# Kernel tuning notes

Hardware: AMD Instinct MI355X
Metric: run time of the kernel (lower is better)

Reference implementation:

```python
import jax, jax.numpy as jnp
import numpy as np

HEADS = 8
DIM_HEAD = 64
BATCH = 2  # classifier-free-guidance batch
LORA_SCALE = 1.0


def setup_inputs() -> dict:
    key = jax.random.key(0)
    ks = jax.random.split(key, 14)
    D, R = 512, 4
    BF, N = 32, 1024  # batch*frames, spatial tokens
    g = lambda k, shape, s: jax.random.normal(k, shape, dtype=jnp.float32) * s
    return {
        "hidden_states": g(ks[0], (BF, N, D), 1.0),
        "Wq": g(ks[1], (D, D), 0.02),
        "Wk": g(ks[2], (D, D), 0.02),
        "Wv": g(ks[3], (D, D), 0.02),
        "q_down": g(ks[4], (D, R), 0.25),
        "q_up": g(ks[5], (R, D), 0.02),
        "k_down": g(ks[6], (D, R), 0.25),
        "k_up": g(ks[7], (R, D), 0.02),
        "v_down": g(ks[8], (D, R), 0.25),
        "v_up": g(ks[9], (R, D), 0.02),
        "Wo": g(ks[10], (D, D), 0.02),
        "bo": jnp.zeros((D,), jnp.float32),
        "o_down": g(ks[11], (D, R), 0.25),
        "o_up": g(ks[12], (R, D), 0.02),
    }


def reference(hidden_states, Wq, Wk, Wv, q_down, q_up, k_down, k_up,
              v_down, v_up, Wo, bo, o_down, o_up):
    BF, N, C = hidden_states.shape
    F = BF // BATCH  # video_length
    inner = HEADS * DIM_HEAD

    # LoRA-augmented QKV projections (self-attention: context == hidden_states)
    q = hidden_states @ Wq + LORA_SCALE * ((hidden_states @ q_down) @ q_up)
    k = hidden_states @ Wk + LORA_SCALE * ((hidden_states @ k_down) @ k_up)
    v = hidden_states @ Wv + LORA_SCALE * ((hidden_states @ v_down) @ v_up)

    # previous-frame gather: frame f attends to frame max(f-1, 0)
    prev = jnp.concatenate([jnp.zeros((1,), jnp.int32),
                            jnp.arange(F - 1, dtype=jnp.int32)])
    k = k.reshape(BATCH, F, N, inner)[:, prev].reshape(BF, N, inner)
    v = v.reshape(BATCH, F, N, inner)[:, prev].reshape(BF, N, inner)

    def to_heads(t):  # (BF, N, inner) -> (BF*H, N, dh)
        return t.reshape(BF, N, HEADS, DIM_HEAD).transpose(0, 2, 1, 3)\
                .reshape(BF * HEADS, N, DIM_HEAD)

    qh, kh, vh = to_heads(q), to_heads(k), to_heads(v)

    scores = jnp.einsum('bid,bjd->bij', qh, kh) * (DIM_HEAD ** -0.5)
    probs = jax.nn.softmax(scores, axis=-1)
    h = jnp.einsum('bij,bjd->bid', probs, vh)

    # heads back to channel dim
    h = h.reshape(BF, HEADS, N, DIM_HEAD).transpose(0, 2, 1, 3).reshape(BF, N, inner)

    # output projection (with bias) + LoRA on the pre-projection activations
    return h @ Wo + bo + LORA_SCALE * ((h @ o_down) @ o_up)
```

## Files before the change

### kernel.cpp

```cpp
#include <hip/hip_runtime.h>
#include <hip/hip_bf16.h>
#include <math.h>

#define D512 512
#define NTOK 1024
#define QSCALE 0.1803368801111137f

typedef __attribute__((ext_vector_type(8))) short short8;
typedef __attribute__((ext_vector_type(4))) float f32x4;
typedef __attribute__((ext_vector_type(16))) float f32x16;
typedef __attribute__((ext_vector_type(4))) unsigned int u32x4;
typedef unsigned short ushort;

__device__ inline ushort f2bf(float x) {
    union { float f; unsigned u; } a; a.f = x;
    unsigned r = a.u + 0x7FFF + ((a.u >> 16) & 1);
    return (ushort)(r >> 16);
}

__device__ inline unsigned cvtpk(float a, float b) {
    unsigned r;
    asm volatile("v_cvt_pk_bf16_f32 %0, %1, %2" : "=v"(r) : "v"(a), "v"(b));
    return r;
}

__device__ inline void plswap(unsigned &a, unsigned &b) {
    asm volatile("v_permlane32_swap_b32 %0, %1" : "+v"(a), "+v"(b));
}

#define GLL16(src, dst) __builtin_amdgcn_global_load_lds( \
    (const __attribute__((address_space(1))) unsigned int*)(src), \
    (__attribute__((address_space(3))) unsigned int*)(dst), 16, 0, 0)

__global__ __launch_bounds__(256) void cvt_bf16(
    const float* __restrict__ in, ushort* __restrict__ out)
{
    const int idx = blockIdx.x * 256 + threadIdx.x;
    float4 a = ((const float4*)in)[idx * 2];
    float4 b = ((const float4*)in)[idx * 2 + 1];
    short8 s;
    s[0] = f2bf(a.x); s[1] = f2bf(a.y); s[2] = f2bf(a.z); s[3] = f2bf(a.w);
    s[4] = f2bf(b.x); s[5] = f2bf(b.y); s[6] = f2bf(b.z); s[7] = f2bf(b.w);
    *(short8*)&out[(size_t)idx * 8] = s;
}

__global__ __launch_bounds__(256) void fold_weights_T(
    const float* __restrict__ Wq, const float* __restrict__ Wk,
    const float* __restrict__ Wv, const float* __restrict__ Wo,
    const float* __restrict__ qd, const float* __restrict__ qu,
    const float* __restrict__ kd, const float* __restrict__ ku,
    const float* __restrict__ vd, const float* __restrict__ vu,
    const float* __restrict__ od, const float* __restrict__ ou,
    ushort* __restrict__ out)
{
    const int which = blockIdx.y;
    const float *W, *dn, *up;
    if (which == 0)      { W = Wq; dn = qd; up = qu; }
    else if (which == 1) { W = Wk; dn = kd; up = ku; }
    else if (which == 2) { W = Wv; dn = vd; up = vu; }
    else                 { W = Wo; dn = od; up = ou; }

    const int td = (blockIdx.x >> 3) * 64;
    const int te = (blockIdx.x & 7) * 64;
    __shared__ float T[64][65];
    const int r4 = threadIdx.x >> 6;
    const int c  = threadIdx.x & 63;

    #pragma unroll
    for (int i = 0; i < 16; ++i) {
        int row = i * 4 + r4;
        T[row][c] = W[(size_t)(td + row) * 512 + te + c];
    }
    __syncthreads();
    #pragma unroll
    for (int i = 0; i < 16; ++i) {
        int e = te + i * 4 + r4;
        int d = td + c;
        float s = T[c][i * 4 + r4];
        #pragma unroll
        for (int r = 0; r < 4; ++r) s += dn[d * 4 + r] * up[r * 512 + e];
        out[(size_t)which * 262144 + (size_t)e * 512 + d] = f2bf(s);
    }
}

template<int QKV>
__global__ __launch_bounds__(256) void gemm_mfma(
    const ushort* __restrict__ A, const ushort* __restrict__ BT,
    const float* __restrict__ bias, float* __restrict__ Co,
    ushort* __restrict__ qb, ushort* __restrict__ kb, ushort* __restrict__ vtb)
{
    __shared__ ushort smem[16384];

    const int tid = threadIdx.x;
    const int w = tid >> 6, l = tid & 63;
    const int l15 = l & 15, l4 = l >> 4;

    const int wg = blockIdx.x;
    const int rxcd = wg & 7, t = wg >> 3;
    const int NX = QKV ? 12 : 4;
    const int xb = t % NX, yh = t / NX;
    const int yb = (yh << 3) | rxcd;
    const int m0 = yb * 128;
    const int n0 = xb * 128;

    const int srow = l >> 2;
    const int scol = (l & 3) * 8;
    const ushort* Asrc = A  + (size_t)(m0 + w * 32 + srow) * 512 + scol;
    const ushort* Bsrc = BT + (size_t)(n0 + w * 32 + srow) * 512 + scol;

    const int wm = (w >> 1) * 64, wn = (w & 1) * 64;

    f32x4 acc[4][4] = {};

    {
        ushort* AsW = smem + w * 1024;
        ushort* BsW = smem + 4096 + w * 1024;
        GLL16(Asrc, AsW);            GLL16(Asrc + 16 * 512, AsW + 512);
        GLL16(Bsrc, BsW);            GLL16(Bsrc + 16 * 512, BsW + 512);
    }
    __syncthreads();

    int cur = 0;
    for (int k0 = 0; k0 < 512; k0 += 32) {
        if (k0 < 480) {
            ushort* AsW = smem + (cur ^ 1) * 8192 + w * 1024;
            ushort* BsW = smem + (cur ^ 1) * 8192 + 4096 + w * 1024;
            GLL16(Asrc + k0 + 32, AsW);
            GLL16(Asrc + k0 + 32 + 16 * 512, AsW + 512);
            GLL16(Bsrc + k0 + 32, BsW);
            GLL16(Bsrc + k0 + 32 + 16 * 512, BsW + 512);
        }
        const ushort* As = smem + cur * 8192;
        const ushort* Bs = smem + cur * 8192 + 4096;

        short8 bfr[4];
        #pragma unroll
        for (int ni = 0; ni < 4; ++ni)
            bfr[ni] = *(const short8*)&Bs[(wn + ni * 16 + l15) * 32 + l4 * 8];
        __builtin_amdgcn_s_setprio(1);
        #pragma unroll
        for (int mi = 0; mi < 4; ++mi) {
            short8 af = *(const short8*)&As[(wm + mi * 16 + l15) * 32 + l4 * 8];
            #pragma unroll
            for (int ni = 0; ni < 4; ++ni)
                acc[mi][ni] = __builtin_amdgcn_mfma_f32_16x16x32_bf16(
                    af, bfr[ni], acc[mi][ni], 0, 0, 0);
        }
        __builtin_amdgcn_s_setprio(0);
        __syncthreads();
        cur ^= 1;
    }

    if (QKV) {
        const int which = xb >> 2;
        if (which < 2) {
            const float sc = which ? 1.0f : QSCALE;
            ushort* dst = which ? kb : qb;
            #pragma unroll
            for (int mi = 0; mi < 4; ++mi)
                #pragma unroll
                for (int j = 0; j < 4; ++j) {
                    const int row = m0 + wm + mi * 16 + l4 * 4 + j;
                    #pragma unroll
                    for (int ni = 0; ni < 4; ++ni) {
                        const int col = (n0 & 511) + wn + ni * 16 + l15;
                        size_t off = (((size_t)(row >> 10) * 8 + (col >> 6)) * NTOK
                                      + (row & 1023)) * 64 + (col & 63);
                        dst[off] = f2bf(acc[mi][ni][j] * sc);
                    }
                }
        } else {
            #pragma unroll
            for (int mi = 0; mi < 4; ++mi) {
                const int rowb = m0 + wm + mi * 16 + l4 * 4;
                const int nn = rowb & 1023;
                const int bf8 = (rowb >> 10) * 8;
                #pragma unroll
                for (int ni = 0; ni < 4; ++ni) {
                    const int col = (n0 & 511) + wn + ni * 16 + l15;
                    const int d = col & 63, head = (col >> 6) & 7;
                    unsigned w0 = cvtpk(acc[mi][ni][0], acc[mi][ni][1]);
                    unsigned w1 = cvtpk(acc[mi][ni][2], acc[mi][ni][3]);
                    *(unsigned long long*)&vtb[((size_t)(bf8 + head) * 64 + d) * NTOK + nn] =
                        (unsigned long long)w0 | ((unsigned long long)w1 << 32);
                }
            }
        }
    } else {
        float bvals[4];
        #pragma unroll
        for (int ni = 0; ni < 4; ++ni)
            bvals[ni] = bias[n0 + wn + ni * 16 + l15];
        #pragma unroll
        for (int mi = 0; mi < 4; ++mi)
            #pragma unroll
            for (int j = 0; j < 4; ++j) {
                const int row = m0 + wm + mi * 16 + l4 * 4 + j;
                #pragma unroll
                for (int ni = 0; ni < 4; ++ni) {
                    const int col = n0 + wn + ni * 16 + l15;
                    Co[(size_t)row * 512 + col] = acc[mi][ni][j] + bvals[ni];
                }
            }
    }
}

#define SWZ(r, c) ((((r) * 64) + (c)) ^ (((r) & 7) << 3))

__global__ __launch_bounds__(256, 2) void attn_mfma32(
    const ushort* __restrict__ qb, const ushort* __restrict__ kb,
    const ushort* __restrict__ vtb, ushort* __restrict__ hb)
{
    __shared__ ushort smem[16384];

    const int tid = threadIdx.x;
    const int w = tid >> 6, l = tid & 63;
    const int l31 = l & 31, hi = l >> 5;
    const int lr = l >> 3, lc = l & 7;

    const int wg = blockIdx.x;
    const int rxcd = wg & 7, t = wg >> 3;
    const int qblk = t & 7;
    const int bh = ((t >> 3) << 3) | rxcd;

    const size_t qbase = (size_t)bh * 65536;
    const int src_bh = ((bh >> 3) & 15) ? bh - 8 : bh;
    const size_t kvbase = (size_t)src_bh * 65536;

    const int qrow = qblk * 128 + w * 32 + l31;
    const ushort* qp = qb + qbase + (size_t)qrow * 64 + hi * 8;
    short8 qf[4];
    #pragma unroll
    for (int dq = 0; dq < 4; ++dq) qf[dq] = *(const short8*)(qp + dq * 16);

    f32x16 acc0 = {}, acc1 = {};
    float lsum = 0.f;

    const int r0 = w * 16 + lr;
    const int ck8 = (lc ^ lr) * 8;

#define STAGE_KV(ktv, b) { \
    ushort* KD = smem + (b) * 8192 + w * 1024; \
    ushort* VD = smem + (b) * 8192 + 4096 + w * 1024; \
    GLL16(kb  + kvbase + (size_t)((ktv) * 64 + r0)     * 64 + ck8, KD); \
    GLL16(kb  + kvbase + (size_t)((ktv) * 64 + r0 + 8) * 64 + ck8, KD + 512); \
    GLL16(vtb + kvbase + (size_t)r0       * 1024 + (ktv) * 64 + ck8, VD); \
    GLL16(vtb + kvbase + (size_t)(r0 + 8) * 1024 + (ktv) * 64 + ck8, VD + 512); }

    STAGE_KV(0, 0);
    __syncthreads();

    int cur = 0;
    for (int kt = 0; kt < 16; ++kt) {
        if (kt < 15) STAGE_KV(kt + 1, cur ^ 1);
        const ushort* Ks = smem + cur * 8192;
        const ushort* Vt = smem + cur * 8192 + 4096;

        f32x16 sv0 = {}, sv1 = {};
        __builtin_amdgcn_s_setprio(1);
        #pragma unroll
        for (int dq = 0; dq < 4; ++dq) {
            short8 kf0 = *(const short8*)&Ks[SWZ(l31,      dq * 16 + hi * 8)];
            short8 kf1 = *(const short8*)&Ks[SWZ(32 + l31, dq * 16 + hi * 8)];
            sv0 = __builtin_amdgcn_mfma_f32_32x32x16_bf16(kf0, qf[dq], sv0, 0, 0, 0);
            sv1 = __builtin_amdgcn_mfma_f32_32x32x16_bf16(kf1, qf[dq], sv1, 0, 0, 0);
        }
        __builtin_amdgcn_s_setprio(0);

        unsigned pk[2][4][2];
        float ls = 0.f;
        #pragma unroll
        for (int rq = 0; rq < 4; ++rq) {
            float p0 = __builtin_amdgcn_exp2f(sv0[4 * rq + 0]);
            float p1 = __builtin_amdgcn_exp2f(sv0[4 * rq + 1]);
            float p2 = __builtin_amdgcn_exp2f(sv0[4 * rq + 2]);
            float p3 = __builtin_amdgcn_exp2f(sv0[4 * rq + 3]);
            ls += (p0 + p1) + (p2 + p3);
            pk[0][rq][0] = cvtpk(p0, p1);
            pk[0][rq][1] = cvtpk(p2, p3);
            float q0 = __builtin_amdgcn_exp2f(sv1[4 * rq + 0]);
            float q1 = __builtin_amdgcn_exp2f(sv1[4 * rq + 1]);
            float q2 = __builtin_amdgcn_exp2f(sv1[4 * rq + 2]);
            float q3 = __builtin_amdgcn_exp2f(sv1[4 * rq + 3]);
            ls += (q0 + q1) + (q2 + q3);
            pk[1][rq][0] = cvtpk(q0, q1);
            pk[1][rq][1] = cvtpk(q2, q3);
        }
        lsum += ls;

        union { u32x4 u; short8 s; } pa[4];
        #pragma unroll
        for (int ks = 0; ks < 4; ++ks) {
            const int kt2 = ks >> 1, q2 = ks & 1;
            unsigned a0 = pk[kt2][2 * q2][0], b0 = pk[kt2][2 * q2 + 1][0];
            unsigned a1 = pk[kt2][2 * q2][1], b1 = pk[kt2][2 * q2 + 1][1];
            plswap(a0, b0);
            plswap(a1, b1);
            pa[ks].u[0] = a0; pa[ks].u[1] = a1;
            pa[ks].u[2] = b0; pa[ks].u[3] = b1;
        }

        __builtin_amdgcn_s_setprio(1);
        #pragma unroll
        for (int ks = 0; ks < 4; ++ks) {
            short8 vf0 = *(const short8*)&Vt[SWZ(l31,      ks * 16 + hi * 8)];
            short8 vf1 = *(const short8*)&Vt[SWZ(32 + l31, ks * 16 + hi * 8)];
            acc0 = __builtin_amdgcn_mfma_f32_32x32x16_bf16(vf0, pa[ks].s, acc0, 0, 0, 0);
            acc1 = __builtin_amdgcn_mfma_f32_32x32x16_bf16(vf1, pa[ks].s, acc1, 0, 0, 0);
        }
        __builtin_amdgcn_s_setprio(0);

        __syncthreads();
        cur ^= 1;
    }
#undef STAGE_KV

    {
        unsigned au = __float_as_uint(lsum), bu = au;
        plswap(au, bu);
        lsum = __uint_as_float(au) + __uint_as_float(bu);
    }

    const float inv = 1.f / lsum;
    ushort* tw = smem + w * 2048;
    #pragma unroll
    for (int r = 0; r < 16; ++r) {
        const int d = (r & 3) + 8 * (r >> 2) + 4 * hi;
        tw[SWZ(l31, d)]      = f2bf(acc0[r] * inv);
        tw[SWZ(l31, 32 + d)] = f2bf(acc1[r] * inv);
    }
    const int q2 = l >> 1, ch = (l & 1) * 32;
    const int hrow = qblk * 128 + w * 32 + q2;
    ushort* gdst = hb + ((size_t)(bh >> 3) * NTOK + hrow) * D512 + (bh & 7) * 64 + ch;
    #pragma unroll
    for (int c = 0; c < 4; ++c)
        *(u32x4*)(gdst + c * 8) = *(const u32x4*)&tw[SWZ(q2, ch + c * 8)];
}

extern "C" void kernel_launch(void* const* d_in, const int* in_sizes, int n_in,
                              void* d_out, int out_size, void* d_ws, size_t ws_size,
                              hipStream_t stream)
{
    const float* hs = (const float*)d_in[0];
    const float* Wq = (const float*)d_in[1];
    const float* Wk = (const float*)d_in[2];
    const float* Wv = (const float*)d_in[3];
    const float* qd = (const float*)d_in[4];
    const float* qu = (const float*)d_in[5];
    const float* kd = (const float*)d_in[6];
    const float* ku = (const float*)d_in[7];
    const float* vd = (const float*)d_in[8];
    const float* vu = (const float*)d_in[9];
    const float* Wo = (const float*)d_in[10];
    const float* bo = (const float*)d_in[11];
    const float* od = (const float*)d_in[12];
    const float* ou = (const float*)d_in[13];

    ushort* wsb = (ushort*)d_ws;
    ushort* WT  = wsb;
    ushort* hsb = wsb + 1048576;
    ushort* qb  = hsb + 16777216;
    ushort* kb  = qb  + 16777216;
    ushort* vtb = kb  + 16777216;
    ushort* hbb = vtb + 16777216;

    float* out = (float*)d_out;

    cvt_bf16<<<dim3(8192), 256, 0, stream>>>(hs, hsb);
    fold_weights_T<<<dim3(64, 4), 256, 0, stream>>>(
        Wq, Wk, Wv, Wo, qd, qu, kd, ku, vd, vu, od, ou, WT);

    gemm_mfma<1><<<dim3(3072), 256, 0, stream>>>(
        hsb, WT, nullptr, nullptr, qb, kb, vtb);

    attn_mfma32<<<dim3(2048), 256, 0, stream>>>(qb, kb, vtb, hbb);

    gemm_mfma<0><<<dim3(1024), 256, 0, stream>>>(
        hbb, WT + 786432, bo, out, nullptr, nullptr, nullptr);
}
```

Measured before the change: 207.7 us.

## Process two 128-row query blocks per attention workgroup to reuse staged K/V

Each attention workgroup now handles 256 query rows, as two 128-row halves, instead of 128. The K/V tiles staged in LDS and the fragments read from them are shared by both halves, which halves global K/V traffic and the LDS fragment loads per query row. The grid drops from 2048 to 1024 workgroups. In exchange, register pressure roughly doubles for the accumulators and score tiles, which could spill or cut occupancy under launch_bounds(256,2), and the smaller grid leaves fewer waves to hide latency.

```diff
diff --git a/kernel.cpp b/kernel.cpp
--- a/kernel.cpp
+++ b/kernel.cpp
@@ -207,6 +207,38 @@
 
 #define SWZ(r, c) ((((r) * 64) + (c)) ^ (((r) & 7) << 3))
 
+#define SOFTPACK(sv0, sv1, lsum, pa) { \
+    unsigned pk[2][4][2]; \
+    float ls = 0.f; \
+    _Pragma("unroll") \
+    for (int rq = 0; rq < 4; ++rq) { \
+        float p0 = __builtin_amdgcn_exp2f(sv0[4 * rq + 0]); \
+        float p1 = __builtin_amdgcn_exp2f(sv0[4 * rq + 1]); \
+        float p2 = __builtin_amdgcn_exp2f(sv0[4 * rq + 2]); \
+        float p3 = __builtin_amdgcn_exp2f(sv0[4 * rq + 3]); \
+        ls += (p0 + p1) + (p2 + p3); \
+        pk[0][rq][0] = cvtpk(p0, p1); \
+        pk[0][rq][1] = cvtpk(p2, p3); \
+        float q0 = __builtin_amdgcn_exp2f(sv1[4 * rq + 0]); \
+        float q1 = __builtin_amdgcn_exp2f(sv1[4 * rq + 1]); \
+        float q2 = __builtin_amdgcn_exp2f(sv1[4 * rq + 2]); \
+        float q3 = __builtin_amdgcn_exp2f(sv1[4 * rq + 3]); \
+        ls += (q0 + q1) + (q2 + q3); \
+        pk[1][rq][0] = cvtpk(q0, q1); \
+        pk[1][rq][1] = cvtpk(q2, q3); \
+    } \
+    lsum += ls; \
+    _Pragma("unroll") \
+    for (int ks = 0; ks < 4; ++ks) { \
+        const int kt2 = ks >> 1, q2 = ks & 1; \
+        unsigned a0 = pk[kt2][2 * q2][0], b0 = pk[kt2][2 * q2 + 1][0]; \
+        unsigned a1 = pk[kt2][2 * q2][1], b1 = pk[kt2][2 * q2 + 1][1]; \
+        plswap(a0, b0); \
+        plswap(a1, b1); \
+        pa[ks].u[0] = a0; pa[ks].u[1] = a1; \
+        pa[ks].u[2] = b0; pa[ks].u[3] = b1; \
+    } }
+
 __global__ __launch_bounds__(256, 2) void attn_mfma32(
     const ushort* __restrict__ qb, const ushort* __restrict__ kb,
     const ushort* __restrict__ vtb, ushort* __restrict__ hb)
@@ -220,21 +252,25 @@
 
     const int wg = blockIdx.x;
     const int rxcd = wg & 7, t = wg >> 3;
-    const int qblk = t & 7;
-    const int bh = ((t >> 3) << 3) | rxcd;
+    const int qblk = t & 3;
+    const int bh = ((t >> 2) << 3) | rxcd;
 
     const size_t qbase = (size_t)bh * 65536;
     const int src_bh = ((bh >> 3) & 15) ? bh - 8 : bh;
     const size_t kvbase = (size_t)src_bh * 65536;
 
-    const int qrow = qblk * 128 + w * 32 + l31;
-    const ushort* qp = qb + qbase + (size_t)qrow * 64 + hi * 8;
-    short8 qf[4];
+    const int qrowA = qblk * 256 + w * 32 + l31;
+    const ushort* qpA = qb + qbase + (size_t)qrowA * 64 + hi * 8;
+    const ushort* qpB = qpA + 128 * 64;
+    short8 qfA[4], qfB[4];
     #pragma unroll
-    for (int dq = 0; dq < 4; ++dq) qf[dq] = *(const short8*)(qp + dq * 16);
-
-    f32x16 acc0 = {}, acc1 = {};
-    float lsum = 0.f;
+    for (int dq = 0; dq < 4; ++dq) {
+        qfA[dq] = *(const short8*)(qpA + dq * 16);
+        qfB[dq] = *(const short8*)(qpB + dq * 16);
+    }
+
+    f32x16 accA0 = {}, accA1 = {}, accB0 = {}, accB1 = {};
+    float lsumA = 0.f, lsumB = 0.f;
 
     const int r0 = w * 16 + lr;
     const int ck8 = (lc ^ lr) * 8;
@@ -256,57 +292,32 @@
         const ushort* Ks = smem + cur * 8192;
         const ushort* Vt = smem + cur * 8192 + 4096;
 
-        f32x16 sv0 = {}, sv1 = {};
+        f32x16 svA0 = {}, svA1 = {}, svB0 = {}, svB1 = {};
         __builtin_amdgcn_s_setprio(1);
         #pragma unroll
         for (int dq = 0; dq < 4; ++dq) {
             short8 kf0 = *(const short8*)&Ks[SWZ(l31,      dq * 16 + hi * 8)];
             short8 kf1 = *(const short8*)&Ks[SWZ(32 + l31, dq * 16 + hi * 8)];
-            sv0 = __builtin_amdgcn_mfma_f32_32x32x16_bf16(kf0, qf[dq], sv0, 0, 0, 0);
-            sv1 = __builtin_amdgcn_mfma_f32_32x32x16_bf16(kf1, qf[dq], sv1, 0, 0, 0);
+            svA0 = __builtin_amdgcn_mfma_f32_32x32x16_bf16(kf0, qfA[dq], svA0, 0, 0, 0);
+            svA1 = __builtin_amdgcn_mfma_f32_32x32x16_bf16(kf1, qfA[dq], svA1, 0, 0, 0);
+            svB0 = __builtin_amdgcn_mfma_f32_32x32x16_bf16(kf0, qfB[dq], svB0, 0, 0, 0);
+            svB1 = __builtin_amdgcn_mfma_f32_32x32x16_bf16(kf1, qfB[dq], svB1, 0, 0, 0);
         }
         __builtin_amdgcn_s_setprio(0);
 
-        unsigned pk[2][4][2];
-        float ls = 0.f;
-        #pragma unroll
-        for (int rq = 0; rq < 4; ++rq) {
-            float p0 = __builtin_amdgcn_exp2f(sv0[4 * rq + 0]);
-            float p1 = __builtin_amdgcn_exp2f(sv0[4 * rq + 1]);
-            float p2 = __builtin_amdgcn_exp2f(sv0[4 * rq + 2]);
-            float p3 = __builtin_amdgcn_exp2f(sv0[4 * rq + 3]);
-            ls += (p0 + p1) + (p2 + p3);
-            pk[0][rq][0] = cvtpk(p0, p1);
-            pk[0][rq][1] = cvtpk(p2, p3);
-            float q0 = __builtin_amdgcn_exp2f(sv1[4 * rq + 0]);
-            float q1 = __builtin_amdgcn_exp2f(sv1[4 * rq + 1]);
-            float q2 = __builtin_amdgcn_exp2f(sv1[4 * rq + 2]);
-            float q3 = __builtin_amdgcn_exp2f(sv1[4 * rq + 3]);
-            ls += (q0 + q1) + (q2 + q3);
-            pk[1][rq][0] = cvtpk(q0, q1);
-            pk[1][rq][1] = cvtpk(q2, q3);
-        }
-        lsum += ls;
-
-        union { u32x4 u; short8 s; } pa[4];
-        #pragma unroll
-        for (int ks = 0; ks < 4; ++ks) {
-            const int kt2 = ks >> 1, q2 = ks & 1;
-            unsigned a0 = pk[kt2][2 * q2][0], b0 = pk[kt2][2 * q2 + 1][0];
-            unsigned a1 = pk[kt2][2 * q2][1], b1 = pk[kt2][2 * q2 + 1][1];
-            plswap(a0, b0);
-            plswap(a1, b1);
-            pa[ks].u[0] = a0; pa[ks].u[1] = a1;
-            pa[ks].u[2] = b0; pa[ks].u[3] = b1;
-        }
+        union { u32x4 u; short8 s; } paA[4], paB[4];
+        SOFTPACK(svA0, svA1, lsumA, paA);
+        SOFTPACK(svB0, svB1, lsumB, paB);
 
         __builtin_amdgcn_s_setprio(1);
         #pragma unroll
         for (int ks = 0; ks < 4; ++ks) {
             short8 vf0 = *(const short8*)&Vt[SWZ(l31,      ks * 16 + hi * 8)];
             short8 vf1 = *(const short8*)&Vt[SWZ(32 + l31, ks * 16 + hi * 8)];
-            acc0 = __builtin_amdgcn_mfma_f32_32x32x16_bf16(vf0, pa[ks].s, acc0, 0, 0, 0);
-            acc1 = __builtin_amdgcn_mfma_f32_32x32x16_bf16(vf1, pa[ks].s, acc1, 0, 0, 0);
+            accA0 = __builtin_amdgcn_mfma_f32_32x32x16_bf16(vf0, paA[ks].s, accA0, 0, 0, 0);
+            accA1 = __builtin_amdgcn_mfma_f32_32x32x16_bf16(vf1, paA[ks].s, accA1, 0, 0, 0);
+            accB0 = __builtin_amdgcn_mfma_f32_32x32x16_bf16(vf0, paB[ks].s, accB0, 0, 0, 0);
+            accB1 = __builtin_amdgcn_mfma_f32_32x32x16_bf16(vf1, paB[ks].s, accB1, 0, 0, 0);
         }
         __builtin_amdgcn_s_setprio(0);
 
@@ -316,25 +327,45 @@
 #undef STAGE_KV
 
     {
-        unsigned au = __float_as_uint(lsum), bu = au;
+        unsigned au = __float_as_uint(lsumA), bu = au;
         plswap(au, bu);
-        lsum = __uint_as_float(au) + __uint_as_float(bu);
-    }
-
-    const float inv = 1.f / lsum;
+        lsumA = __uint_as_float(au) + __uint_as_float(bu);
+        unsigned cu2 = __float_as_uint(lsumB), du = cu2;
+        plswap(cu2, du);
+        lsumB = __uint_as_float(cu2) + __uint_as_float(du);
+    }
+
     ushort* tw = smem + w * 2048;
-    #pragma unroll
-    for (int r = 0; r < 16; ++r) {
-        const int d = (r & 3) + 8 * (r >> 2) + 4 * hi;
-        tw[SWZ(l31, d)]      = f2bf(acc0[r] * inv);
-        tw[SWZ(l31, 32 + d)] = f2bf(acc1[r] * inv);
-    }
     const int q2 = l >> 1, ch = (l & 1) * 32;
-    const int hrow = qblk * 128 + w * 32 + q2;
-    ushort* gdst = hb + ((size_t)(bh >> 3) * NTOK + hrow) * D512 + (bh & 7) * 64 + ch;
-    #pragma unroll
-    for (int c = 0; c < 4; ++c)
-        *(u32x4*)(gdst + c * 8) = *(const u32x4*)&tw[SWZ(q2, ch + c * 8)];
+    {
+        const float inv = 1.f / lsumA;
+        #pragma unroll
+        for (int r = 0; r < 16; ++r) {
+            const int d = (r & 3) + 8 * (r >> 2) + 4 * hi;
+            tw[SWZ(l31, d)]      = f2bf(accA0[r] * inv);
+            tw[SWZ(l31, 32 + d)] = f2bf(accA1[r] * inv);
+        }
+        const int hrow = qblk * 256 + w * 32 + q2;
+        ushort* gdst = hb + ((size_t)(bh >> 3) * NTOK + hrow) * D512 + (bh & 7) * 64 + ch;
+        #pragma unroll
+        for (int c = 0; c < 4; ++c)
+            *(u32x4*)(gdst + c * 8) = *(const u32x4*)&tw[SWZ(q2, ch + c * 8)];
+    }
+    __builtin_amdgcn_s_waitcnt(0);
+    {
+        const float inv = 1.f / lsumB;
+        #pragma unroll
+        for (int r = 0; r < 16; ++r) {
+            const int d = (r & 3) + 8 * (r >> 2) + 4 * hi;
+            tw[SWZ(l31, d)]      = f2bf(accB0[r] * inv);
+            tw[SWZ(l31, 32 + d)] = f2bf(accB1[r] * inv);
+        }
+        const int hrow = qblk * 256 + 128 + w * 32 + q2;
+        ushort* gdst = hb + ((size_t)(bh >> 3) * NTOK + hrow) * D512 + (bh & 7) * 64 + ch;
+        #pragma unroll
+        for (int c = 0; c < 4; ++c)
+            *(u32x4*)(gdst + c * 8) = *(const u32x4*)&tw[SWZ(q2, ch + c * 8)];
+    }
 }
 
 extern "C" void kernel_launch(void* const* d_in, const int* in_sizes, int n_in,
@@ -373,7 +404,7 @@
     gemm_mfma<1><<<dim3(3072), 256, 0, stream>>>(
         hsb, WT, nullptr, nullptr, qb, kb, vtb);
 
-    attn_mfma32<<<dim3(2048), 256, 0, stream>>>(qb, kb, vtb, hbb);
+    attn_mfma32<<<dim3(1024), 256, 0, stream>>>(qb, kb, vtb, hbb);
 
     gemm_mfma<0><<<dim3(1024), 256, 0, stream>>>(
         hbb, WT + 786432, bo, out, nullptr, nullptr, nullptr);
```

New measurement: 200.5 us. -3.4%, faster.
